# Performance work log

Hardware: AMD Instinct MI355X
Metric: run time of the kernel (lower is better)

The kernel has to match this reference:

```python
import jax, jax.numpy as jnp
import numpy as np

C = 128      # c_in
H = 4        # no_heads
DH = 32      # c_hidden // no_heads (per-head dim)
INF = 1e9
EPS = 1e-5


def setup_inputs() -> dict:
    key = jax.random.key(0)
    ks = jax.random.split(key, 10)
    B, I, J = 1, 384, 384
    x = jax.random.normal(ks[0], (B, I, J, C), dtype=jnp.float32)
    mask = jnp.ones((B, I, J), dtype=jnp.float32)
    s = 0.02
    return {
        "x": x,
        "mask": mask,
        "ln_w": jnp.ones((C,), jnp.float32),
        "ln_b": jnp.zeros((C,), jnp.float32),
        "w_tri": jax.random.normal(ks[1], (C, H), jnp.float32) * s,   # bias=False
        "wq": jax.random.normal(ks[2], (C, H * DH), jnp.float32) * s,
        "wk": jax.random.normal(ks[3], (C, H * DH), jnp.float32) * s,
        "wv": jax.random.normal(ks[4], (C, H * DH), jnp.float32) * s,
        "wg": jax.random.normal(ks[5], (C, H * DH), jnp.float32) * s,
        "bg": jnp.zeros((H * DH,), jnp.float32),
        "wo": jax.random.normal(ks[6], (H * DH, C), jnp.float32) * s,
        "bo": jnp.zeros((C,), jnp.float32),
    }


def reference(x, mask, ln_w, ln_b, w_tri, wq, wk, wv, wg, bg, wo, bo):
    # starting=True: attend along rows (J axis), no transpose.
    B, I, J, _ = x.shape
    # LayerNorm over channel dim
    mu = jnp.mean(x, axis=-1, keepdims=True)
    var = jnp.mean(jnp.square(x - mu), axis=-1, keepdims=True)
    xn = (x - mu) * jax.lax.rsqrt(var + EPS) * ln_w + ln_b

    # mask bias: [B, I, 1, 1, J]
    mask_bias = (INF * (mask - 1.0))[:, :, None, None, :]
    # triangle bias: linear -> [B, I, J, H] -> permute (2,0,1) -> [B, H, I, J] -> [B, 1, H, I, J]
    tri = jnp.einsum('bijc,ch->bhij', xn, w_tri)[:, None]

    # multi-head attention with gating (OpenFold-style), batch dims (B, I), seq J
    q = jnp.einsum('bijc,cf->bijf', xn, wq).reshape(B, I, J, H, DH)
    k = jnp.einsum('bijc,cf->bijf', xn, wk).reshape(B, I, J, H, DH)
    v = jnp.einsum('bijc,cf->bijf', xn, wv).reshape(B, I, J, H, DH)
    q = q / np.sqrt(DH).astype(np.float32)

    # scores: [B, I, H, Q, K] + mask bias + triangle bias
    scores = jnp.einsum('biqhd,bikhd->bihqk', q, k) + mask_bias + tri
    a = jax.nn.softmax(scores, axis=-1)
    o = jnp.einsum('bihqk,bikhd->biqhd', a, v).reshape(B, I, J, H * DH)

    g = jax.nn.sigmoid(jnp.einsum('bijc,cf->bijf', xn, wg) + bg)
    o = o * g
    out = jnp.einsum('bijf,fc->bijc', o, wo) + bo
    return out
```

## Files before the change

kernel.cpp:

```cpp
#include <hip/hip_runtime.h>
#include <hip/hip_bf16.h>

#define NPOS (384*384)
#define JDIM 384
#define CDIM 128
#define HNUM 4
#define DHD  32

typedef __attribute__((ext_vector_type(8))) short short8;
typedef __attribute__((ext_vector_type(4))) float floatx4;
typedef unsigned short ushort_t;

__device__ __forceinline__ float bf2f(unsigned short u){
  unsigned int x = ((unsigned int)u) << 16;
  return __builtin_bit_cast(float, x);
}
__device__ __forceinline__ unsigned short f2bf(float f){
  unsigned int u = __builtin_bit_cast(unsigned int, f);
  u = u + 0x7FFFu + ((u >> 16) & 1u);
  return (unsigned short)(u >> 16);
}
__device__ __forceinline__ unsigned int pack2bf(float a, float b){
  unsigned int ua = __builtin_bit_cast(unsigned int, a);
  unsigned int ub = __builtin_bit_cast(unsigned int, b);
  ua = ua + 0x7FFFu + ((ua >> 16) & 1u);
  ub = ub + 0x7FFFu + ((ub >> 16) & 1u);
  return __builtin_amdgcn_perm(ub, ua, 0x07060302);
}

__global__ __launch_bounds__(256) void ln_tri_kernel(
    const float* __restrict__ x, const float* __restrict__ lnw,
    const float* __restrict__ lnb, const float* __restrict__ wtri,
    ushort_t* __restrict__ xn, float* __restrict__ trip)
{
  int wave = threadIdx.x >> 6, lane = threadIdx.x & 63;
  int pos = blockIdx.x * 4 + wave;
  const float2 xv = *(const float2*)(x + (size_t)pos*CDIM + lane*2);
  float x0 = xv.x, x1 = xv.y;
  float s = x0 + x1, ss = x0*x0 + x1*x1;
  #pragma unroll
  for (int o = 32; o > 0; o >>= 1){ s += __shfl_xor(s, o); ss += __shfl_xor(ss, o); }
  float mu  = s * (1.0f/128.0f);
  float var = ss * (1.0f/128.0f) - mu*mu;
  float rstd = rsqrtf(var + 1e-5f);
  float2 w2 = *(const float2*)(lnw + lane*2);
  float2 b2 = *(const float2*)(lnb + lane*2);
  float n0 = (x0 - mu)*rstd*w2.x + b2.x;
  float n1 = (x1 - mu)*rstd*w2.y + b2.y;
  ushort2 o2; o2.x = f2bf(n0); o2.y = f2bf(n1);
  *(ushort2*)(xn + (size_t)pos*CDIM + lane*2) = o2;
  float4 wt0 = *(const float4*)(wtri + lane*8);
  float4 wt1 = *(const float4*)(wtri + lane*8 + 4);
  float t0 = n0*wt0.x + n1*wt1.x;
  float t1 = n0*wt0.y + n1*wt1.y;
  float t2 = n0*wt0.z + n1*wt1.z;
  float t3 = n0*wt0.w + n1*wt1.w;
  #pragma unroll
  for (int o = 32; o > 0; o >>= 1){
    t0 += __shfl_xor(t0, o); t1 += __shfl_xor(t1, o);
    t2 += __shfl_xor(t2, o); t3 += __shfl_xor(t3, o);
  }
  if (lane == 0){
    trip[0*NPOS + pos] = t0;
    trip[1*NPOS + pos] = t1;
    trip[2*NPOS + pos] = t2;
    trip[3*NPOS + pos] = t3;
  }
}

__global__ __launch_bounds__(256) void wt_kernel(
    const float* wq, const float* wk, const float* wv,
    const float* wg, const float* wo, ushort_t* __restrict__ wt)
{
  int mat = blockIdx.x >> 6;
  int idx = ((blockIdx.x & 63) << 8) | threadIdx.x;
  const float* src = (mat==0)?wq:(mat==1)?wk:(mat==2)?wv:(mat==3)?wg:wo;
  int f = idx >> 7, c = idx & 127;
  wt[mat*16384 + idx] = f2bf(src[c*128 + f]);
}

__device__ __forceinline__ void gemm_body(
    const ushort_t* __restrict__ A, const ushort_t* __restrict__ W,
    void* __restrict__ outv, const float* __restrict__ bias,
    int mode, int row0, ushort_t* As, ushort_t* Bs)
{
  int t = threadIdx.x;
  #pragma unroll
  for (int i = 0; i < 8; i++){
    int v = t + i*256;
    int row = v >> 4, c8 = v & 15;
    *(short8*)(As + row*144 + c8*8) = *(const short8*)(A + (size_t)(row0+row)*CDIM + c8*8);
    *(short8*)(Bs + row*144 + c8*8) = *(const short8*)(W + v*8);
  }
  __syncthreads();
  int w = t >> 6, lane = t & 63;
  int wm = (w & 1) * 64, wn = (w >> 1) * 64;
  int m = lane & 15, q4 = lane >> 4;
  floatx4 acc[4][4];
  #pragma unroll
  for (int mi = 0; mi < 4; mi++)
    #pragma unroll
    for (int ni = 0; ni < 4; ni++)
      acc[mi][ni] = (floatx4){0.f, 0.f, 0.f, 0.f};
  #pragma unroll
  for (int k0 = 0; k0 < 128; k0 += 32){
    int koff = k0 + q4*8;
    short8 af[4], bf[4];
    #pragma unroll
    for (int mi = 0; mi < 4; mi++) af[mi] = *(const short8*)(As + (wm + mi*16 + m)*144 + koff);
    #pragma unroll
    for (int ni = 0; ni < 4; ni++) bf[ni] = *(const short8*)(Bs + (wn + ni*16 + m)*144 + koff);
    #pragma unroll
    for (int mi = 0; mi < 4; mi++)
      #pragma unroll
      for (int ni = 0; ni < 4; ni++)
        acc[mi][ni] = __builtin_amdgcn_mfma_f32_16x16x32_bf16(af[mi], bf[ni], acc[mi][ni], 0, 0, 0);
  }
  const float scale = 0.17677669529663687f;
  #pragma unroll
  for (int mi = 0; mi < 4; mi++){
    #pragma unroll
    for (int ni = 0; ni < 4; ni++){
      int col = wn + ni*16 + m;
      float bv = (mode >= 2) ? bias[col] : 0.f;
      #pragma unroll
      for (int r = 0; r < 4; r++){
        float val = acc[mi][ni][r];
        if (mode == 1) val *= scale;
        else if (mode == 2) val = 1.f / (1.f + __expf(-(val + bv)));
        else if (mode == 3) val += bv;
        int row = wm + mi*16 + q4*4 + r;
        size_t oidx = (size_t)(row0+row)*CDIM + col;
        if (mode == 3) ((float*)outv)[oidx] = val;
        else           ((ushort_t*)outv)[oidx] = f2bf(val);
      }
    }
  }
}

__global__ __launch_bounds__(256) void proj_gemm_kernel(
    const ushort_t* __restrict__ xn, const ushort_t* __restrict__ wt,
    ushort_t* __restrict__ outb, const float* __restrict__ bg)
{
  __shared__ __align__(16) ushort_t As[128*144];
  __shared__ __align__(16) ushort_t Bs[128*144];
  int proj = blockIdx.y;
  int mode = (proj == 0) ? 1 : (proj == 3) ? 2 : 0;
  gemm_body(xn, wt + proj*16384, outb + (size_t)proj*NPOS*CDIM, bg, mode,
            blockIdx.x * 128, As, Bs);
}

__global__ __launch_bounds__(256) void out_gemm_kernel(
    const ushort_t* __restrict__ og, const ushort_t* __restrict__ wt,
    float* __restrict__ out, const float* __restrict__ bo)
{
  __shared__ __align__(16) ushort_t As[128*144];
  __shared__ __align__(16) ushort_t Bs[128*144];
  gemm_body(og, wt, (void*)out, bo, 3, blockIdx.x * 128, As, Bs);
}

#define VT_STRIDE 392
#define P_STRIDE  40
__global__ __launch_bounds__(256, 2) void attn_kernel(
    const ushort_t* __restrict__ qb, const ushort_t* __restrict__ kb,
    const ushort_t* __restrict__ vb, const ushort_t* __restrict__ gb,
    const float* __restrict__ mask, const float* __restrict__ trip,
    ushort_t* __restrict__ og)
{
  __shared__ __align__(16) ushort_t Ks[JDIM*32];
  __shared__ __align__(16) ushort_t Vt[32*VT_STRIDE];
  __shared__ __align__(16) ushort_t Pb[4*96*P_STRIDE];
  int i = blockIdx.x, h = blockIdx.y;
  int t = threadIdx.x;
  size_t rbase = (size_t)i * JDIM;

  for (int idx = t; idx < JDIM*4; idx += 256){
    int j = idx >> 2, c8 = idx & 3;
    *(short8*)(Ks + j*32 + c8*8) = *(const short8*)(kb + (rbase + j)*CDIM + h*DHD + c8*8);
    short8 v8 = *(const short8*)(vb + (rbase + j)*CDIM + h*DHD + c8*8);
    int jb = j & 31;
    int jp = (j & ~31) | (((jb & 15) << 1) | (jb >> 4));
    #pragma unroll
    for (int e = 0; e < 8; e++) Vt[(c8*8 + e)*VT_STRIDE + jp] = (unsigned short)v8[e];
  }
  __syncthreads();

  int w = t >> 6, lane = t & 63;
  int m = lane & 15, q4 = lane >> 4;
  int wm = w * 96;
  ushort_t* Pw = Pb + w * 96 * P_STRIDE;

  short8 qf[6];
  #pragma unroll
  for (int t6 = 0; t6 < 6; t6++)
    qf[t6] = *(const short8*)(qb + (rbase + wm + t6*16 + m)*CDIM + h*DHD + q4*8);

  floatx4 oacc[6][2];
  float lpart[6][4];
  #pragma unroll
  for (int t6 = 0; t6 < 6; t6++){
    oacc[t6][0] = (floatx4){0.f,0.f,0.f,0.f};
    oacc[t6][1] = (floatx4){0.f,0.f,0.f,0.f};
    #pragma unroll
    for (int r = 0; r < 4; r++) lpart[t6][r] = 0.f;
  }

  const float* triph = trip + (size_t)h * NPOS;

  for (int kbk = 0; kbk < 12; kbk++){
    int col0 = kbk * 32;
    short8 kf0 = *(const short8*)(Ks + (col0 + m)*32 + q4*8);
    short8 kf1 = *(const short8*)(Ks + (col0 + 16 + m)*32 + q4*8);
    float mb0 = 1e9f * (mask[rbase + col0 + m] - 1.0f);
    float mb1 = 1e9f * (mask[rbase + col0 + 16 + m] - 1.0f);

    #pragma unroll
    for (int t6 = 0; t6 < 6; t6++){
      floatx4 z = (floatx4){0.f,0.f,0.f,0.f};
      floatx4 s0 = __builtin_amdgcn_mfma_f32_16x16x32_bf16(qf[t6], kf0, z, 0, 0, 0);
      floatx4 s1 = __builtin_amdgcn_mfma_f32_16x16x32_bf16(qf[t6], kf1, z, 0, 0, 0);
      int qrow = wm + t6*16 + q4*4;
      #pragma unroll
      for (int r = 0; r < 4; r++){
        const float* trow = triph + (size_t)(qrow + r)*JDIM + col0;
        float sc0 = s0[r] + mb0 + trow[m];
        float sc1 = s1[r] + mb1 + trow[16 + m];
        float p0 = __expf(sc0);
        float p1 = __expf(sc1);
        lpart[t6][r] += p0 + p1;
        *(unsigned int*)(Pw + (t6*16 + q4*4 + r)*P_STRIDE + m*2) = pack2bf(p0, p1);
      }
    }
    short8 vf0 = *(const short8*)(Vt + m*VT_STRIDE + col0 + q4*8);
    short8 vf1 = *(const short8*)(Vt + (16 + m)*VT_STRIDE + col0 + q4*8);
    #pragma unroll
    for (int t6 = 0; t6 < 6; t6++){
      short8 pf = *(const short8*)(Pw + (t6*16 + m)*P_STRIDE + q4*8);
      oacc[t6][0] = __builtin_amdgcn_mfma_f32_16x16x32_bf16(pf, vf0, oacc[t6][0], 0, 0, 0);
      oacc[t6][1] = __builtin_amdgcn_mfma_f32_16x16x32_bf16(pf, vf1, oacc[t6][1], 0, 0, 0);
    }
  }

  #pragma unroll
  for (int t6 = 0; t6 < 6; t6++)
    #pragma unroll
    for (int r = 0; r < 4; r++){
      float l = lpart[t6][r];
      l += __shfl_xor(l, 1); l += __shfl_xor(l, 2);
      l += __shfl_xor(l, 4); l += __shfl_xor(l, 8);
      lpart[t6][r] = 1.0f / (l + 1e-30f);
    }

  #pragma unroll
  for (int t6 = 0; t6 < 6; t6++){
    int qrow = wm + t6*16 + q4*4;
    #pragma unroll
    for (int dt = 0; dt < 2; dt++){
      #pragma unroll
      for (int r = 0; r < 4; r++){
        size_t oidx = (rbase + qrow + r)*CDIM + h*DHD + dt*16 + m;
        float o = oacc[t6][dt][r] * lpart[t6][r] * bf2f(gb[oidx]);
        og[oidx] = f2bf(o);
      }
    }
  }
}

extern "C" void kernel_launch(void* const* d_in, const int* in_sizes, int n_in,
                              void* d_out, int out_size, void* d_ws, size_t ws_size,
                              hipStream_t stream)
{
  const float* x    = (const float*)d_in[0];
  const float* mask = (const float*)d_in[1];
  const float* lnw  = (const float*)d_in[2];
  const float* lnb  = (const float*)d_in[3];
  const float* wtri = (const float*)d_in[4];
  const float* wq   = (const float*)d_in[5];
  const float* wk   = (const float*)d_in[6];
  const float* wv   = (const float*)d_in[7];
  const float* wg   = (const float*)d_in[8];
  const float* bg   = (const float*)d_in[9];
  const float* wo   = (const float*)d_in[10];
  const float* bo   = (const float*)d_in[11];

  char* ws = (char*)d_ws;
  const size_t SZ = (size_t)NPOS * CDIM * 2;
  ushort_t* xn  = (ushort_t*)(ws);
  ushort_t* qb  = (ushort_t*)(ws + 1*SZ);
  ushort_t* kbp = (ushort_t*)(ws + 2*SZ);
  ushort_t* vbp = (ushort_t*)(ws + 3*SZ);
  ushort_t* gbp = (ushort_t*)(ws + 4*SZ);
  ushort_t* og  = (ushort_t*)(ws + 5*SZ);
  ushort_t* wt  = (ushort_t*)(ws + 6*SZ);
  float*    tri = (float*)(ws + 6*SZ + 5*16384*2);

  ln_tri_kernel<<<NPOS/4, 256, 0, stream>>>(x, lnw, lnb, wtri, xn, tri);
  wt_kernel<<<320, 256, 0, stream>>>(wq, wk, wv, wg, wo, wt);
  proj_gemm_kernel<<<dim3(NPOS/128, 4), 256, 0, stream>>>(xn, wt, qb, bg);
  attn_kernel<<<dim3(JDIM, HNUM), 256, 0, stream>>>(qb, kbp, vbp, gbp, mask, tri, og);
  out_gemm_kernel<<<NPOS/128, 256, 0, stream>>>(og, wt + 4*16384, (float*)d_out, bo);
}
```

Before: 387.7 us.

## Use exp2 softmax, transposed tri-bias loaded into MFMA accumulator, 512-thread attention blocks

The log2(e) factor is folded into the q scale, the triangle bias and the mask bias so the softmax can call a native exp2 instead of __expf. The triangle bias is now stored transposed so each lane loads four contiguous query rows as a float4 and seeds the MFMA accumulator with bias plus mask, removing the strided scalar loads and separate adds. Probability packing uses the hardware v_cvt_pk_bf16_f32 instruction. The attention block doubles to 512 threads with 48 query rows per wave, cutting per-wave register use and raising the number of waves in flight. The transposed stores in ln_tri are scattered, which makes that kernel's writes less coalesced.

```diff
diff --git a/kernel.cpp b/kernel.cpp
--- a/kernel.cpp
+++ b/kernel.cpp
@@ -7,9 +7,17 @@
 #define HNUM 4
 #define DHD  32
 
+#define LOG2E 1.4426950408889634f
+
 typedef __attribute__((ext_vector_type(8))) short short8;
 typedef __attribute__((ext_vector_type(4))) float floatx4;
 typedef unsigned short ushort_t;
+
+#if __has_builtin(__builtin_amdgcn_exp2f)
+#define EXP2F(x) __builtin_amdgcn_exp2f(x)
+#else
+#define EXP2F(x) exp2f(x)
+#endif
 
 __device__ __forceinline__ float bf2f(unsigned short u){
   unsigned int x = ((unsigned int)u) << 16;
@@ -20,12 +28,10 @@
   u = u + 0x7FFFu + ((u >> 16) & 1u);
   return (unsigned short)(u >> 16);
 }
-__device__ __forceinline__ unsigned int pack2bf(float a, float b){
-  unsigned int ua = __builtin_bit_cast(unsigned int, a);
-  unsigned int ub = __builtin_bit_cast(unsigned int, b);
-  ua = ua + 0x7FFFu + ((ua >> 16) & 1u);
-  ub = ub + 0x7FFFu + ((ub >> 16) & 1u);
-  return __builtin_amdgcn_perm(ub, ua, 0x07060302);
+__device__ __forceinline__ unsigned int cvtpk_bf16(float a, float b){
+  unsigned int r;
+  asm("v_cvt_pk_bf16_f32 %0, %1, %2" : "=v"(r) : "v"(a), "v"(b));
+  return r;
 }
 
 __global__ __launch_bounds__(256) void ln_tri_kernel(
@@ -61,10 +67,13 @@
     t2 += __shfl_xor(t2, o); t3 += __shfl_xor(t3, o);
   }
   if (lane == 0){
-    trip[0*NPOS + pos] = t0;
-    trip[1*NPOS + pos] = t1;
-    trip[2*NPOS + pos] = t2;
-    trip[3*NPOS + pos] = t3;
+    int i = pos / JDIM;
+    int j = pos - i*JDIM;
+    int tp = j*JDIM + i;
+    trip[0*NPOS + tp] = t0 * LOG2E;
+    trip[1*NPOS + tp] = t1 * LOG2E;
+    trip[2*NPOS + tp] = t2 * LOG2E;
+    trip[3*NPOS + tp] = t3 * LOG2E;
   }
 }
 
@@ -116,7 +125,7 @@
       for (int ni = 0; ni < 4; ni++)
         acc[mi][ni] = __builtin_amdgcn_mfma_f32_16x16x32_bf16(af[mi], bf[ni], acc[mi][ni], 0, 0, 0);
   }
-  const float scale = 0.17677669529663687f;
+  const float scale = 0.17677669529663687f * LOG2E;
   #pragma unroll
   for (int mi = 0; mi < 4; mi++){
     #pragma unroll
@@ -161,7 +170,7 @@
 
 #define VT_STRIDE 392
 #define P_STRIDE  40
-__global__ __launch_bounds__(256, 2) void attn_kernel(
+__global__ __launch_bounds__(512, 4) void attn_kernel(
     const ushort_t* __restrict__ qb, const ushort_t* __restrict__ kb,
     const ushort_t* __restrict__ vb, const ushort_t* __restrict__ gb,
     const float* __restrict__ mask, const float* __restrict__ trip,
@@ -169,12 +178,12 @@
 {
   __shared__ __align__(16) ushort_t Ks[JDIM*32];
   __shared__ __align__(16) ushort_t Vt[32*VT_STRIDE];
-  __shared__ __align__(16) ushort_t Pb[4*96*P_STRIDE];
+  __shared__ __align__(16) ushort_t Pb[8*48*P_STRIDE];
   int i = blockIdx.x, h = blockIdx.y;
   int t = threadIdx.x;
   size_t rbase = (size_t)i * JDIM;
 
-  for (int idx = t; idx < JDIM*4; idx += 256){
+  for (int idx = t; idx < JDIM*4; idx += 512){
     int j = idx >> 2, c8 = idx & 3;
     *(short8*)(Ks + j*32 + c8*8) = *(const short8*)(kb + (rbase + j)*CDIM + h*DHD + c8*8);
     short8 v8 = *(const short8*)(vb + (rbase + j)*CDIM + h*DHD + c8*8);
@@ -187,18 +196,18 @@
 
   int w = t >> 6, lane = t & 63;
   int m = lane & 15, q4 = lane >> 4;
-  int wm = w * 96;
-  ushort_t* Pw = Pb + w * 96 * P_STRIDE;
-
-  short8 qf[6];
-  #pragma unroll
-  for (int t6 = 0; t6 < 6; t6++)
+  int wm = w * 48;
+  ushort_t* Pw = Pb + w * 48 * P_STRIDE;
+
+  short8 qf[3];
+  #pragma unroll
+  for (int t6 = 0; t6 < 3; t6++)
     qf[t6] = *(const short8*)(qb + (rbase + wm + t6*16 + m)*CDIM + h*DHD + q4*8);
 
-  floatx4 oacc[6][2];
-  float lpart[6][4];
-  #pragma unroll
-  for (int t6 = 0; t6 < 6; t6++){
+  floatx4 oacc[3][2];
+  float lpart[3][4];
+  #pragma unroll
+  for (int t6 = 0; t6 < 3; t6++){
     oacc[t6][0] = (floatx4){0.f,0.f,0.f,0.f};
     oacc[t6][1] = (floatx4){0.f,0.f,0.f,0.f};
     #pragma unroll
@@ -211,30 +220,30 @@
     int col0 = kbk * 32;
     short8 kf0 = *(const short8*)(Ks + (col0 + m)*32 + q4*8);
     short8 kf1 = *(const short8*)(Ks + (col0 + 16 + m)*32 + q4*8);
-    float mb0 = 1e9f * (mask[rbase + col0 + m] - 1.0f);
-    float mb1 = 1e9f * (mask[rbase + col0 + 16 + m] - 1.0f);
-
-    #pragma unroll
-    for (int t6 = 0; t6 < 6; t6++){
-      floatx4 z = (floatx4){0.f,0.f,0.f,0.f};
-      floatx4 s0 = __builtin_amdgcn_mfma_f32_16x16x32_bf16(qf[t6], kf0, z, 0, 0, 0);
-      floatx4 s1 = __builtin_amdgcn_mfma_f32_16x16x32_bf16(qf[t6], kf1, z, 0, 0, 0);
-      int qrow = wm + t6*16 + q4*4;
+    float mb0 = (1e9f*LOG2E) * (mask[rbase + col0 + m] - 1.0f);
+    float mb1 = (1e9f*LOG2E) * (mask[rbase + col0 + 16 + m] - 1.0f);
+
+    #pragma unroll
+    for (int t6 = 0; t6 < 3; t6++){
+      int qrow0 = wm + t6*16 + q4*4;
+      float4 tt0 = *(const float4*)(triph + (size_t)(col0 + m)*JDIM + qrow0);
+      float4 tt1 = *(const float4*)(triph + (size_t)(col0 + 16 + m)*JDIM + qrow0);
+      floatx4 z0 = (floatx4){tt0.x + mb0, tt0.y + mb0, tt0.z + mb0, tt0.w + mb0};
+      floatx4 z1 = (floatx4){tt1.x + mb1, tt1.y + mb1, tt1.z + mb1, tt1.w + mb1};
+      floatx4 s0 = __builtin_amdgcn_mfma_f32_16x16x32_bf16(qf[t6], kf0, z0, 0, 0, 0);
+      floatx4 s1 = __builtin_amdgcn_mfma_f32_16x16x32_bf16(qf[t6], kf1, z1, 0, 0, 0);
       #pragma unroll
       for (int r = 0; r < 4; r++){
-        const float* trow = triph + (size_t)(qrow + r)*JDIM + col0;
-        float sc0 = s0[r] + mb0 + trow[m];
-        float sc1 = s1[r] + mb1 + trow[16 + m];
-        float p0 = __expf(sc0);
-        float p1 = __expf(sc1);
+        float p0 = EXP2F(s0[r]);
+        float p1 = EXP2F(s1[r]);
         lpart[t6][r] += p0 + p1;
-        *(unsigned int*)(Pw + (t6*16 + q4*4 + r)*P_STRIDE + m*2) = pack2bf(p0, p1);
+        *(unsigned int*)(Pw + (t6*16 + q4*4 + r)*P_STRIDE + m*2) = cvtpk_bf16(p0, p1);
       }
     }
     short8 vf0 = *(const short8*)(Vt + m*VT_STRIDE + col0 + q4*8);
     short8 vf1 = *(const short8*)(Vt + (16 + m)*VT_STRIDE + col0 + q4*8);
     #pragma unroll
-    for (int t6 = 0; t6 < 6; t6++){
+    for (int t6 = 0; t6 < 3; t6++){
       short8 pf = *(const short8*)(Pw + (t6*16 + m)*P_STRIDE + q4*8);
       oacc[t6][0] = __builtin_amdgcn_mfma_f32_16x16x32_bf16(pf, vf0, oacc[t6][0], 0, 0, 0);
       oacc[t6][1] = __builtin_amdgcn_mfma_f32_16x16x32_bf16(pf, vf1, oacc[t6][1], 0, 0, 0);
@@ -242,7 +251,7 @@
   }
 
   #pragma unroll
-  for (int t6 = 0; t6 < 6; t6++)
+  for (int t6 = 0; t6 < 3; t6++)
     #pragma unroll
     for (int r = 0; r < 4; r++){
       float l = lpart[t6][r];
@@ -252,7 +261,7 @@
     }
 
   #pragma unroll
-  for (int t6 = 0; t6 < 6; t6++){
+  for (int t6 = 0; t6 < 3; t6++){
     int qrow = wm + t6*16 + q4*4;
     #pragma unroll
     for (int dt = 0; dt < 2; dt++){
@@ -297,6 +306,6 @@
   ln_tri_kernel<<<NPOS/4, 256, 0, stream>>>(x, lnw, lnb, wtri, xn, tri);
   wt_kernel<<<320, 256, 0, stream>>>(wq, wk, wv, wg, wo, wt);
   proj_gemm_kernel<<<dim3(NPOS/128, 4), 256, 0, stream>>>(xn, wt, qb, bg);
-  attn_kernel<<<dim3(JDIM, HNUM), 256, 0, stream>>>(qb, kbp, vbp, gbp, mask, tri, og);
+  attn_kernel<<<dim3(JDIM, HNUM), 512, 0, stream>>>(qb, kbp, vbp, gbp, mask, tri, og);
   out_gemm_kernel<<<NPOS/128, 256, 0, stream>>>(og, wt + 4*16384, (float*)d_out, bo);
 }
```

Measured after the change: 391.3 us. Within noise of the previous version (+0.9%).
